# Kernel optimization log

Hardware: AMD Instinct MI355X
Metric: run time of the kernel (lower is better)

The kernel has to match this reference:

```python
import jax, jax.numpy as jnp
import numpy as np

K = 16            # neighbors
QUERY_CHUNK = 256 # SE is applied per chunk of this many query points (matches torch loop)
EPS = 1e-5        # BatchNorm eps (eval mode, running stats)


def bn(x, g, b, m, v):
    # eval-mode batchnorm over last axis (channel-last layout here)
    return (x - m) * (g / jnp.sqrt(v + EPS)) + b


def setup_inputs() -> dict:
    key = jax.random.key(0)
    ks = jax.random.split(key, 16)
    B, Cin, N = 4, 128, 4096
    H, Cout = 128, 256
    se_h = Cout // 4
    r = lambda k, s, sc=1.0: jax.random.normal(k, s, jnp.float32) * sc
    return dict(
        x=r(ks[0], (B, Cin, N)),
        W_edge=r(ks[1], (H, 2 * Cin), 0.05),          # edge_mlp conv2d 1x1
        bn1_g=jnp.ones((H,), jnp.float32), bn1_b=jnp.zeros((H,), jnp.float32),
        bn1_m=r(ks[2], (H,), 0.1), bn1_v=jax.random.uniform(ks[3], (H,), jnp.float32) + 0.5,
        w_att=r(ks[4], (H,), 0.1),                     # att_conv (1,H,1,1)
        W_fuse=r(ks[5], (Cout, H), 0.05),              # fuse conv1d
        bn2_g=jnp.ones((Cout,), jnp.float32), bn2_b=jnp.zeros((Cout,), jnp.float32),
        bn2_m=r(ks[6], (Cout,), 0.1), bn2_v=jax.random.uniform(ks[7], (Cout,), jnp.float32) + 0.5,
        fc1_w=r(ks[8], (se_h, Cout), 0.05), fc1_b=jnp.zeros((se_h,), jnp.float32),
        fc2_w=r(ks[9], (Cout, se_h), 0.05), fc2_b=jnp.zeros((Cout,), jnp.float32),
        W_res=r(ks[10], (Cout, Cin), 0.05),            # res_conv conv1d (in!=out)
        bn3_g=jnp.ones((Cout,), jnp.float32), bn3_b=jnp.zeros((Cout,), jnp.float32),
        bn3_m=r(ks[11], (Cout,), 0.1), bn3_v=jax.random.uniform(ks[12], (Cout,), jnp.float32) + 0.5,
    )


def reference(x, W_edge, bn1_g, bn1_b, bn1_m, bn1_v, w_att,
              W_fuse, bn2_g, bn2_b, bn2_m, bn2_v,
              fc1_w, fc1_b, fc2_w, fc2_b,
              W_res, bn3_g, bn3_b, bn3_m, bn3_v):
    B, Cin, N = x.shape
    x_t = jnp.swapaxes(x, 1, 2)  # (B,N,Cin)

    # KNN on features (dynamic=False -> knn on x.transpose); squared euclidean
    # has the same ordering as torch.cdist(p=2).
    sq = jnp.sum(x_t * x_t, axis=-1)                               # (B,N)
    d2 = sq[:, :, None] + sq[:, None, :] - 2.0 * jnp.einsum('bnc,bmc->bnm', x_t, x_t)
    _, idx = jax.lax.top_k(-d2, K)                                  # (B,N,K) smallest dists

    neigh = jax.vmap(lambda p, i: p[i])(x_t, idx)                   # (B,N,K,Cin)
    center = jnp.broadcast_to(x_t[:, :, None, :], neigh.shape)      # (B,N,K,Cin)
    edge = jnp.concatenate([neigh - center, center], axis=-1)       # (B,N,K,2Cin)

    # edge_mlp: 1x1 conv + BN + ReLU
    h = jax.nn.relu(bn(jnp.einsum('bnkc,hc->bnkh', edge, W_edge),
                       bn1_g, bn1_b, bn1_m, bn1_v))                 # (B,N,K,H)

    # attention over neighbors
    att = jax.nn.softmax(jnp.einsum('bnkh,h->bnk', h, w_att), axis=-1)
    agg = jnp.einsum('bnkh,bnk->bnh', h, att)                       # (B,N,H)

    # fuse conv1d + BN + ReLU
    out = jax.nn.relu(bn(jnp.einsum('bnh,oh->bno', agg, W_fuse),
                         bn2_g, bn2_b, bn2_m, bn2_v))               # (B,N,Cout)

    # SE channel attention, applied per query chunk (matches torch loop semantics)
    Cout = out.shape[-1]
    nc = N // QUERY_CHUNK
    oc = out.reshape(B, nc, QUERY_CHUNK, Cout)
    s = oc.mean(axis=2)                                             # (B,nc,Cout)
    s = jax.nn.relu(jnp.einsum('bmc,hc->bmh', s, fc1_w) + fc1_b)
    s = jax.nn.sigmoid(jnp.einsum('bmh,ch->bmc', s, fc2_w) + fc2_b)
    out = (oc * s[:, :, None, :]).reshape(B, N, Cout)

    # residual projection (in_channels != out_channels)
    res = bn(jnp.einsum('bnc,oc->bno', x_t, W_res), bn3_g, bn3_b, bn3_m, bn3_v)
    out = out + res
    return jnp.swapaxes(out, 1, 2)                                  # (B,Cout,N)
```

## Files before the change

kernel.cpp:

```cpp
#include <hip/hip_runtime.h>
#include <cstddef>

typedef __bf16 bf16;
typedef __bf16 bf16x8 __attribute__((ext_vector_type(8)));
typedef float  f32x4  __attribute__((ext_vector_type(4)));
typedef unsigned short u16;
typedef unsigned long long u64;

#define MFMA16x16(a, b, c) __builtin_amdgcn_mfma_f32_16x16x32_bf16((a), (b), (c), 0, 0, 0)

namespace {
constexpr int BB   = 4;
constexpr int CIN  = 128;
constexpr int NPT  = 4096;
constexpr int KNBR = 16;
constexpr int HED  = 128;
constexpr int COUT = 256;
}

__device__ __forceinline__ unsigned int ord_f32(float f) {
  unsigned int b = __float_as_uint(f);
  return b ^ (0x80000000u | (unsigned int)((int)b >> 31));
}
__device__ __forceinline__ u64 mk_key(float d, int m) {
  return ((u64)ord_f32(d) << 32) | (unsigned int)m;
}

__device__ __forceinline__ void sort16(u64* k) {
  #pragma unroll
  for (int sz = 2; sz <= 16; sz <<= 1) {
    #pragma unroll
    for (int st = sz >> 1; st > 0; st >>= 1) {
      #pragma unroll
      for (int i = 0; i < 16; ++i) {
        const int j = i ^ st;
        if (j > i) {
          const bool up = ((i & sz) == 0);
          const u64 a = k[i], c = k[j];
          const bool sw = up ? (a > c) : (a < c);
          k[i] = sw ? c : a;
          k[j] = sw ? a : c;
        }
      }
    }
  }
}

__device__ __forceinline__ void merge16(u64* R, const u64* B) {
  u64 t[16];
  #pragma unroll
  for (int i = 0; i < 16; ++i) {
    const u64 a = R[i], c = B[15 - i];
    t[i] = (a < c) ? a : c;
  }
  #pragma unroll
  for (int st = 8; st > 0; st >>= 1) {
    #pragma unroll
    for (int i = 0; i < 16; ++i) {
      const int j = i ^ st;
      if (j > i) {
        const u64 a = t[i], c = t[j];
        const bool sw = a > c;
        t[i] = sw ? c : a;
        t[j] = sw ? a : c;
      }
    }
  }
  #pragma unroll
  for (int i = 0; i < 16; ++i) R[i] = t[i];
}

__global__ __launch_bounds__(256) void k_wconv(const float* __restrict__ We,
                                               const float* __restrict__ Wf,
                                               const float* __restrict__ Wr,
                                               bf16* __restrict__ Web,
                                               bf16* __restrict__ Wfb,
                                               bf16* __restrict__ Wrb) {
  const int i = blockIdx.x * 256 + threadIdx.x;
  const int a = i >> 15;
  const int j = i & 32767;
  const float* src = (a == 0) ? We : (a == 1) ? Wf : Wr;
  bf16*        dst = (a == 0) ? Web : (a == 1) ? Wfb : Wrb;
  dst[j] = (bf16)src[j];
}

__global__ __launch_bounds__(256) void k_prep(const float* __restrict__ x,
                                              bf16* __restrict__ xh,
                                              bf16* __restrict__ xl,
                                              float* __restrict__ sq) {
  __shared__ __attribute__((aligned(16))) bf16 th[64][136];
  __shared__ __attribute__((aligned(16))) bf16 tl[64][136];
  __shared__ float sqp[4][64];
  const int tid = threadIdx.x;
  const int b   = blockIdx.x >> 6;
  const int n0  = (blockIdx.x & 63) << 6;
  const int nl  = tid & 63;
  const int cg  = tid >> 6;
  const float* xb = x + (size_t)b * CIN * NPT;
  float acc = 0.f;
  #pragma unroll
  for (int rep = 0; rep < 32; ++rep) {
    const int c = rep * 4 + cg;
    const float v = xb[(size_t)c * NPT + n0 + nl];
    const bf16 h = (bf16)v;
    const bf16 l = (bf16)(v - (float)h);
    acc += v * v;
    th[nl][c] = h;
    tl[nl][c] = l;
  }
  sqp[cg][nl] = acc;
  __syncthreads();
  bf16* xho = xh + ((size_t)b * NPT + n0) * CIN;
  bf16* xlo = xl + ((size_t)b * NPT + n0) * CIN;
  #pragma unroll
  for (int rep = 0; rep < 32; ++rep) {
    const int e = rep * 256 + tid;
    const int r = e >> 7;
    const int c = e & 127;
    xho[(size_t)r * CIN + c] = th[r][c];
    xlo[(size_t)r * CIN + c] = tl[r][c];
  }
  if (tid < 64) {
    sq[b * NPT + n0 + tid] = sqp[0][tid] + sqp[1][tid] + sqp[2][tid] + sqp[3][tid];
  }
}

__global__ __launch_bounds__(256, 2) void k_knn(const bf16* __restrict__ xh,
                                                const bf16* __restrict__ xl,
                                                const float* __restrict__ sq,
                                                int* __restrict__ knn_idx) {
  __shared__ u64 Lk[32][258];
  const int tid  = threadIdx.x;
  const int w    = tid >> 6;
  const int lane = tid & 63;
  const int col  = lane & 15;
  const int quad = lane >> 4;
  const int b    = blockIdx.x >> 7;
  const int q0   = (blockIdx.x & 127) << 5;
  const bf16*  xhb = xh + (size_t)b * NPT * CIN;
  const bf16*  xlb = xl + (size_t)b * NPT * CIN;
  const float* sqb = sq + b * NPT;

  bf16x8 qh[2][4], ql[2][4];
  float sqn[2];
  #pragma unroll
  for (int t = 0; t < 2; ++t) {
    const bf16* qrh = xhb + (size_t)(q0 + t * 16 + col) * CIN + quad * 8;
    const bf16* qrl = xlb + (size_t)(q0 + t * 16 + col) * CIN + quad * 8;
    #pragma unroll
    for (int ks = 0; ks < 4; ++ks) {
      qh[t][ks] = *(const bf16x8*)(qrh + ks * 32);
      ql[t][ks] = *(const bf16x8*)(qrl + ks * 32);
    }
    sqn[t] = sqb[q0 + t * 16 + col];
  }

  u64 R0[16], R1[16];
  #pragma unroll
  for (int i = 0; i < 16; ++i) { R0[i] = ~0ull; R1[i] = ~0ull; }

  const int cbase = w << 10;
  for (int mt = 0; mt < 16; ++mt) {
    const int m0 = cbase + (mt << 6);
    u64 k0[16], k1[16];
    #pragma unroll
    for (int cb = 0; cb < 4; ++cb) {
      const bf16* crh = xhb + (size_t)(m0 + cb * 16 + col) * CIN + quad * 8;
      const bf16* crl = xlb + (size_t)(m0 + cb * 16 + col) * CIN + quad * 8;
      f32x4 a0 = {0.f, 0.f, 0.f, 0.f};
      f32x4 a1 = {0.f, 0.f, 0.f, 0.f};
      #pragma unroll
      for (int ks = 0; ks < 4; ++ks) {
        const bf16x8 ch_ = *(const bf16x8*)(crh + ks * 32);
        const bf16x8 cl_ = *(const bf16x8*)(crl + ks * 32);
        a0 = MFMA16x16(cl_, qh[0][ks], a0);
        a0 = MFMA16x16(ch_, ql[0][ks], a0);
        a0 = MFMA16x16(ch_, qh[0][ks], a0);
        a1 = MFMA16x16(cl_, qh[1][ks], a1);
        a1 = MFMA16x16(ch_, ql[1][ks], a1);
        a1 = MFMA16x16(ch_, qh[1][ks], a1);
      }
      const f32x4 sqm = *(const f32x4*)(sqb + m0 + cb * 16 + quad * 4);
      #pragma unroll
      for (int r = 0; r < 4; ++r) {
        const int m = m0 + cb * 16 + quad * 4 + r;
        k0[cb * 4 + r] = mk_key((sqn[0] + sqm[r]) - 2.0f * a0[r], m);
        k1[cb * 4 + r] = mk_key((sqn[1] + sqm[r]) - 2.0f * a1[r], m);
      }
    }
    sort16(k0); merge16(R0, k0);
    sort16(k1); merge16(R1, k1);
  }

  {
    const int run = (w << 2) | quad;
    const int qA = col;
    const int qB = 16 | col;
    #pragma unroll
    for (int i = 0; i < 16; ++i) {
      Lk[qA][run * 16 + i] = R0[i];
      Lk[qB][run * 16 + i] = R1[i];
    }
  }
  __syncthreads();

  #pragma unroll
  for (int half = 8; half >= 1; half >>= 1) {
    u64 A[16], Bv[16];
    const bool act = tid < 32 * half;
    const int q = tid / half;
    const int j = tid % half;
    if (act) {
      #pragma unroll
      for (int i = 0; i < 16; ++i) {
        A[i]  = Lk[q][(2 * j) * 16 + i];
        Bv[i] = Lk[q][(2 * j + 1) * 16 + i];
      }
    }
    __syncthreads();
    if (act) {
      merge16(A, Bv);
      #pragma unroll
      for (int i = 0; i < 16; ++i) Lk[q][j * 16 + i] = A[i];
    }
    __syncthreads();
  }

  if (tid < 32) {
    int* op = knn_idx + (size_t)(b * NPT + q0 + tid) * KNBR;
    #pragma unroll
    for (int i = 0; i < 16; ++i) op[i] = (int)(Lk[tid][i] & 0xFFFFFFFFull);
  }
}

__global__ __launch_bounds__(256) void k_edge(const bf16* __restrict__ xh,
                                              const bf16* __restrict__ xl,
                                              const int* __restrict__ knn_idx,
                                              const bf16* __restrict__ We,
                                              const float* __restrict__ g1, const float* __restrict__ b1,
                                              const float* __restrict__ m1, const float* __restrict__ v1,
                                              const float* __restrict__ watt,
                                              bf16* __restrict__ agg) {
  __shared__ __attribute__((aligned(16))) bf16 Ew[4][16][264];
  __shared__ float s1[HED], t1[HED], wat[HED];
  const int tid  = threadIdx.x;
  const int w    = tid >> 6;
  const int lane = tid & 63;
  const int col  = lane & 15;
  const int quad = lane >> 4;
  if (tid < HED) {
    const float ss = g1[tid] / sqrtf(v1[tid] + 1e-5f);
    s1[tid] = ss;
    t1[tid] = b1[tid] - m1[tid] * ss;
    wat[tid] = watt[tid];
  }
  __syncthreads();
  const int gw = blockIdx.x * 4 + w;
  for (int it = 0; it < 4; ++it) {
    const int p = gw * 4 + it;
    const int b = p >> 12;
    const int n = p & 4095;
    const bf16* xhb = xh + (size_t)b * NPT * CIN;
    const bf16* xlb = xl + (size_t)b * NPT * CIN;
    const int my = knn_idx[(size_t)p * KNBR + col];
    const int m  = __shfl(my, lane >> 2);
    const int sub = lane & 3;
    const int kn  = lane >> 2;
    const bf16* nh = xhb + (size_t)m * CIN + sub * 32;
    const bf16* nl_ = xlb + (size_t)m * CIN + sub * 32;
    const bf16* ch = xhb + (size_t)n * CIN + sub * 32;
    const bf16* cl = xlb + (size_t)n * CIN + sub * 32;
    #pragma unroll
    for (int j = 0; j < 4; ++j) {
      const bf16x8 nhv = *(const bf16x8*)(nh + j * 8);
      const bf16x8 nlv = *(const bf16x8*)(nl_ + j * 8);
      const bf16x8 chv = *(const bf16x8*)(ch + j * 8);
      const bf16x8 clv = *(const bf16x8*)(cl + j * 8);
      bf16x8 dv, cv;
      #pragma unroll
      for (int e = 0; e < 8; ++e) {
        const float nf = (float)nhv[e] + (float)nlv[e];
        const float cf = (float)chv[e] + (float)clv[e];
        dv[e] = (bf16)(nf - cf);
        cv[e] = (bf16)cf;
      }
      *(bf16x8*)&Ew[w][kn][sub * 32 + j * 8]       = dv;
      *(bf16x8*)&Ew[w][kn][128 + sub * 32 + j * 8] = cv;
    }
    __syncthreads();
    const f32x4 zero4 = {0.f, 0.f, 0.f, 0.f};
    f32x4 acc[8];
    #pragma unroll
    for (int hb = 0; hb < 8; ++hb) acc[hb] = zero4;
    #pragma unroll
    for (int ks = 0; ks < 8; ++ks) {
      const bf16x8 af = *(const bf16x8*)&Ew[w][col][ks * 32 + quad * 8];
      #pragma unroll
      for (int hb = 0; hb < 8; ++hb) {
        const bf16x8 bfv = *(const bf16x8*)(We + (size_t)(hb * 16 + col) * 256 + ks * 32 + quad * 8);
        acc[hb] = MFMA16x16(af, bfv, acc[hb]);
      }
    }
    float h[8][4];
    float lg[4] = {0.f, 0.f, 0.f, 0.f};
    #pragma unroll
    for (int hb = 0; hb < 8; ++hb) {
      const int hc = hb * 16 + col;
      const float ss = s1[hc], tt = t1[hc], ww = wat[hc];
      #pragma unroll
      for (int r = 0; r < 4; ++r) {
        const float hv = fmaxf(acc[hb][r] * ss + tt, 0.f);
        h[hb][r] = hv;
        lg[r] += hv * ww;
      }
    }
    #pragma unroll
    for (int r = 0; r < 4; ++r) {
      float vv = lg[r];
      vv += __shfl_xor(vv, 1);
      vv += __shfl_xor(vv, 2);
      vv += __shfl_xor(vv, 4);
      vv += __shfl_xor(vv, 8);
      lg[r] = vv;
    }
    float mx = fmaxf(fmaxf(lg[0], lg[1]), fmaxf(lg[2], lg[3]));
    mx = fmaxf(mx, __shfl_xor(mx, 16));
    mx = fmaxf(mx, __shfl_xor(mx, 32));
    float ex[4];
    float sm = 0.f;
    #pragma unroll
    for (int r = 0; r < 4; ++r) { ex[r] = expf(lg[r] - mx); sm += ex[r]; }
    sm += __shfl_xor(sm, 16);
    sm += __shfl_xor(sm, 32);
    const float inv = 1.0f / sm;
    float ag[8];
    #pragma unroll
    for (int hb = 0; hb < 8; ++hb) {
      float a = h[hb][0] * ex[0] + h[hb][1] * ex[1] + h[hb][2] * ex[2] + h[hb][3] * ex[3];
      a += __shfl_xor(a, 16);
      a += __shfl_xor(a, 32);
      ag[hb] = a * inv;
    }
    if (quad == 0) {
      bf16* ao = agg + (size_t)p * HED;
      #pragma unroll
      for (int hb = 0; hb < 8; ++hb) ao[hb * 16 + col] = (bf16)ag[hb];
    }
    __syncthreads();
  }
}

__global__ __launch_bounds__(256) void k_fuse(const bf16* __restrict__ agg,
                                              const bf16* __restrict__ Wf,
                                              const float* __restrict__ g2, const float* __restrict__ b2,
                                              const float* __restrict__ m2, const float* __restrict__ v2,
                                              bf16* __restrict__ outp) {
  const int tid  = threadIdx.x;
  const int w    = tid >> 6;
  const int lane = tid & 63;
  const int col  = lane & 15;
  const int quad = lane >> 4;
  const int p0   = (blockIdx.x * 4 + w) * 16;
  bf16x8 afr[4];
  const bf16* arow = agg + (size_t)(p0 + col) * HED + quad * 8;
  #pragma unroll
  for (int ks = 0; ks < 4; ++ks) afr[ks] = *(const bf16x8*)(arow + ks * 32);
  #pragma unroll
  for (int ob = 0; ob < 16; ++ob) {
    f32x4 acc = {0.f, 0.f, 0.f, 0.f};
    const bf16* brow = Wf + (size_t)(ob * 16 + col) * HED + quad * 8;
    #pragma unroll
    for (int ks = 0; ks < 4; ++ks)
      acc = MFMA16x16(afr[ks], *(const bf16x8*)(brow + ks * 32), acc);
    const int o = ob * 16 + col;
    const float ss = g2[o] / sqrtf(v2[o] + 1e-5f);
    const float tt = b2[o] - m2[o] * ss;
    #pragma unroll
    for (int r = 0; r < 4; ++r) {
      outp[(size_t)(p0 + quad * 4 + r) * COUT + o] = (bf16)fmaxf(acc[r] * ss + tt, 0.f);
    }
  }
}

__global__ __launch_bounds__(256) void k_se(const bf16* __restrict__ outp,
                                            const float* __restrict__ f1w, const float* __restrict__ f1b,
                                            const float* __restrict__ f2w, const float* __restrict__ f2b,
                                            float* __restrict__ sse) {
  __shared__ float mean_s[COUT];
  __shared__ float h1[64];
  const int bc  = blockIdx.x;
  const int tid = threadIdx.x;
  const bf16* base = outp + (size_t)bc * 256 * COUT;
  float s = 0.f;
  for (int p2 = 0; p2 < 256; ++p2) s += (float)base[(size_t)p2 * COUT + tid];
  mean_s[tid] = s * (1.0f / 256.0f);
  __syncthreads();
  if (tid < 64) {
    float a = f1b[tid];
    for (int c = 0; c < COUT; ++c) a += f1w[tid * COUT + c] * mean_s[c];
    h1[tid] = fmaxf(a, 0.f);
  }
  __syncthreads();
  float a = f2b[tid];
  #pragma unroll
  for (int j = 0; j < 64; ++j) a += f2w[tid * 64 + j] * h1[j];
  sse[(size_t)bc * COUT + tid] = 1.0f / (1.0f + expf(-a));
}

__global__ __launch_bounds__(256) void k_final(const bf16* __restrict__ xh,
                                               const bf16* __restrict__ Wr,
                                               const float* __restrict__ g3, const float* __restrict__ b3,
                                               const float* __restrict__ m3, const float* __restrict__ v3,
                                               const bf16* __restrict__ outp,
                                               const float* __restrict__ sse,
                                               float* __restrict__ out) {
  const int tid  = threadIdx.x;
  const int w    = tid >> 6;
  const int lane = tid & 63;
  const int col  = lane & 15;
  const int quad = lane >> 4;
  const int p0   = (blockIdx.x * 4 + w) * 16;
  const int b    = p0 >> 12;
  const int n0l  = p0 & 4095;
  bf16x8 afr[4];
  const bf16* arow = xh + (size_t)(p0 + col) * CIN + quad * 8;
  #pragma unroll
  for (int ks = 0; ks < 4; ++ks) afr[ks] = *(const bf16x8*)(arow + ks * 32);
  const float* scb = sse + (size_t)(b * 16 + (n0l >> 8)) * COUT;
  #pragma unroll
  for (int ob = 0; ob < 16; ++ob) {
    f32x4 acc = {0.f, 0.f, 0.f, 0.f};
    const bf16* brow = Wr + (size_t)(ob * 16 + col) * CIN + quad * 8;
    #pragma unroll
    for (int ks = 0; ks < 4; ++ks)
      acc = MFMA16x16(afr[ks], *(const bf16x8*)(brow + ks * 32), acc);
    const int o = ob * 16 + col;
    const float ss = g3[o] / sqrtf(v3[o] + 1e-5f);
    const float tt = b3[o] - m3[o] * ss;
    const float sc = scb[o];
    f32x4 pk;
    #pragma unroll
    for (int r = 0; r < 4; ++r) {
      const float res = acc[r] * ss + tt;
      pk[r] = (float)outp[(size_t)(p0 + quad * 4 + r) * COUT + o] * sc + res;
    }
    float* op = out + (size_t)(b * COUT + o) * NPT + n0l + quad * 4;
    *(f32x4*)op = pk;
  }
}

extern "C" void kernel_launch(void* const* d_in, const int* in_sizes, int n_in,
                              void* d_out, int out_size, void* d_ws, size_t ws_size,
                              hipStream_t stream) {
  (void)in_sizes; (void)n_in; (void)out_size; (void)ws_size;
  const float* x    = (const float*)d_in[0];
  const float* We   = (const float*)d_in[1];
  const float* g1   = (const float*)d_in[2];
  const float* b1   = (const float*)d_in[3];
  const float* m1   = (const float*)d_in[4];
  const float* v1   = (const float*)d_in[5];
  const float* watt = (const float*)d_in[6];
  const float* Wf   = (const float*)d_in[7];
  const float* g2   = (const float*)d_in[8];
  const float* b2   = (const float*)d_in[9];
  const float* m2   = (const float*)d_in[10];
  const float* v2   = (const float*)d_in[11];
  const float* f1w  = (const float*)d_in[12];
  const float* f1b  = (const float*)d_in[13];
  const float* f2w  = (const float*)d_in[14];
  const float* f2b  = (const float*)d_in[15];
  const float* Wr   = (const float*)d_in[16];
  const float* g3   = (const float*)d_in[17];
  const float* b3   = (const float*)d_in[18];
  const float* m3   = (const float*)d_in[19];
  const float* v3   = (const float*)d_in[20];

  char* ws = (char*)d_ws;
  size_t off = 0;
  bf16*  xth  = (bf16*)(ws + off);  off += (size_t)BB * NPT * CIN * 2;
  bf16*  xtl  = (bf16*)(ws + off);  off += (size_t)BB * NPT * CIN * 2;
  float* sq   = (float*)(ws + off); off += (size_t)BB * NPT * 4;
  int*   idxp = (int*)(ws + off);   off += (size_t)BB * NPT * KNBR * 4;
  bf16*  aggp = (bf16*)(ws + off);  off += (size_t)BB * NPT * HED * 2;
  bf16*  outp = (bf16*)(ws + off);  off += (size_t)BB * NPT * COUT * 2;
  float* ssep = (float*)(ws + off); off += (size_t)BB * 16 * COUT * 4;
  bf16*  Web  = (bf16*)(ws + off);  off += (size_t)HED * 2 * CIN * 2;
  bf16*  Wfb  = (bf16*)(ws + off);  off += (size_t)COUT * HED * 2;
  bf16*  Wrb  = (bf16*)(ws + off);  off += (size_t)COUT * CIN * 2;

  float* out = (float*)d_out;

  k_wconv<<<384, 256, 0, stream>>>(We, Wf, Wr, Web, Wfb, Wrb);
  k_prep<<<256, 256, 0, stream>>>(x, xth, xtl, sq);
  k_knn<<<512, 256, 0, stream>>>(xth, xtl, sq, idxp);
  k_edge<<<1024, 256, 0, stream>>>(xth, xtl, idxp, Web, g1, b1, m1, v1, watt, aggp);
  k_fuse<<<256, 256, 0, stream>>>(aggp, Wfb, g2, b2, m2, v2, outp);
  k_se<<<64, 256, 0, stream>>>(outp, f1w, f1b, f2w, f2b, ssep);
  k_final<<<256, 256, 0, stream>>>(xth, Wrb, g3, b3, m3, v3, outp, ssep, out);
}
```

Before: 430.0 us.

## Merge KNN runs via wave shuffles and build edge MFMA fragments in registers

In the KNN kernel, the per-lane top-16 lists are now merged across quads with cross-lane shuffles instead of through shared memory. The shared buffer shrinks to one run per wave, so the final block-level merge becomes a single serial pass by 32 threads with no repeated barriers. Launch bounds rise to 4 blocks per CU, and the first tile initialises the running list directly instead of merging against sentinels. In the edge kernel, the gathered edge features are loaded straight into MFMA A-fragment registers, which removes the shared staging buffer and its barriers but raises register pressure and makes neighbour loads less coalesced.

Result: slower. 727.1 us (+69.1%).

```diff
diff --git a/kernel.cpp b/kernel.cpp
--- a/kernel.cpp
+++ b/kernel.cpp
@@ -125,11 +125,11 @@
   }
 }
 
-__global__ __launch_bounds__(256, 2) void k_knn(const bf16* __restrict__ xh,
+__global__ __launch_bounds__(256, 4) void k_knn(const bf16* __restrict__ xh,
                                                 const bf16* __restrict__ xl,
                                                 const float* __restrict__ sq,
                                                 int* __restrict__ knn_idx) {
-  __shared__ u64 Lk[32][258];
+  __shared__ u64 Lk[32][65];
   const int tid  = threadIdx.x;
   const int w    = tid >> 6;
   const int lane = tid & 63;
@@ -156,9 +156,6 @@
   }
 
   u64 R0[16], R1[16];
-  #pragma unroll
-  for (int i = 0; i < 16; ++i) { R0[i] = ~0ull; R1[i] = ~0ull; }
-
   const int cbase = w << 10;
   for (int mt = 0; mt < 16; ++mt) {
     const int m0 = cbase + (mt << 6);
@@ -188,48 +185,54 @@
         k1[cb * 4 + r] = mk_key((sqn[1] + sqm[r]) - 2.0f * a1[r], m);
       }
     }
-    sort16(k0); merge16(R0, k0);
-    sort16(k1); merge16(R1, k1);
+    sort16(k0);
+    sort16(k1);
+    if (mt == 0) {
+      #pragma unroll
+      for (int i = 0; i < 16; ++i) { R0[i] = k0[i]; R1[i] = k1[i]; }
+    } else {
+      merge16(R0, k0);
+      merge16(R1, k1);
+    }
   }
 
   {
-    const int run = (w << 2) | quad;
-    const int qA = col;
-    const int qB = 16 | col;
+    u64 P[16];
+    #pragma unroll
+    for (int i = 0; i < 16; ++i) P[i] = __shfl_xor((u64)R0[i], 16);
+    merge16(R0, P);
+    #pragma unroll
+    for (int i = 0; i < 16; ++i) P[i] = __shfl_xor((u64)R0[i], 32);
+    merge16(R0, P);
+    #pragma unroll
+    for (int i = 0; i < 16; ++i) P[i] = __shfl_xor((u64)R1[i], 16);
+    merge16(R1, P);
+    #pragma unroll
+    for (int i = 0; i < 16; ++i) P[i] = __shfl_xor((u64)R1[i], 32);
+    merge16(R1, P);
+  }
+  if (quad == 0) {
     #pragma unroll
     for (int i = 0; i < 16; ++i) {
-      Lk[qA][run * 16 + i] = R0[i];
-      Lk[qB][run * 16 + i] = R1[i];
+      Lk[col][w * 16 + i]        = R0[i];
+      Lk[16 | col][w * 16 + i]   = R1[i];
     }
   }
   __syncthreads();
 
-  #pragma unroll
-  for (int half = 8; half >= 1; half >>= 1) {
+  if (tid < 32) {
     u64 A[16], Bv[16];
-    const bool act = tid < 32 * half;
-    const int q = tid / half;
-    const int j = tid % half;
-    if (act) {
-      #pragma unroll
-      for (int i = 0; i < 16; ++i) {
-        A[i]  = Lk[q][(2 * j) * 16 + i];
-        Bv[i] = Lk[q][(2 * j + 1) * 16 + i];
-      }
-    }
-    __syncthreads();
-    if (act) {
+    #pragma unroll
+    for (int i = 0; i < 16; ++i) A[i] = Lk[tid][i];
+    #pragma unroll
+    for (int run = 1; run < 4; ++run) {
+      #pragma unroll
+      for (int i = 0; i < 16; ++i) Bv[i] = Lk[tid][run * 16 + i];
       merge16(A, Bv);
-      #pragma unroll
-      for (int i = 0; i < 16; ++i) Lk[q][j * 16 + i] = A[i];
-    }
-    __syncthreads();
-  }
-
-  if (tid < 32) {
+    }
     int* op = knn_idx + (size_t)(b * NPT + q0 + tid) * KNBR;
     #pragma unroll
-    for (int i = 0; i < 16; ++i) op[i] = (int)(Lk[tid][i] & 0xFFFFFFFFull);
+    for (int i = 0; i < 16; ++i) op[i] = (int)(A[i] & 0xFFFFFFFFull);
   }
 }
 
@@ -241,7 +244,6 @@
                                               const float* __restrict__ m1, const float* __restrict__ v1,
                                               const float* __restrict__ watt,
                                               bf16* __restrict__ agg) {
-  __shared__ __attribute__((aligned(16))) bf16 Ew[4][16][264];
   __shared__ float s1[HED], t1[HED], wat[HED];
   const int tid  = threadIdx.x;
   const int w    = tid >> 6;
@@ -262,20 +264,18 @@
     const int n = p & 4095;
     const bf16* xhb = xh + (size_t)b * NPT * CIN;
     const bf16* xlb = xl + (size_t)b * NPT * CIN;
-    const int my = knn_idx[(size_t)p * KNBR + col];
-    const int m  = __shfl(my, lane >> 2);
-    const int sub = lane & 3;
-    const int kn  = lane >> 2;
-    const bf16* nh = xhb + (size_t)m * CIN + sub * 32;
-    const bf16* nl_ = xlb + (size_t)m * CIN + sub * 32;
-    const bf16* ch = xhb + (size_t)n * CIN + sub * 32;
-    const bf16* cl = xlb + (size_t)n * CIN + sub * 32;
-    #pragma unroll
-    for (int j = 0; j < 4; ++j) {
-      const bf16x8 nhv = *(const bf16x8*)(nh + j * 8);
-      const bf16x8 nlv = *(const bf16x8*)(nl_ + j * 8);
-      const bf16x8 chv = *(const bf16x8*)(ch + j * 8);
-      const bf16x8 clv = *(const bf16x8*)(cl + j * 8);
+    const int m = knn_idx[(size_t)p * KNBR + col];
+    const bf16* nh  = xhb + (size_t)m * CIN + quad * 8;
+    const bf16* nl_ = xlb + (size_t)m * CIN + quad * 8;
+    const bf16* ch  = xhb + (size_t)n * CIN + quad * 8;
+    const bf16* cl  = xlb + (size_t)n * CIN + quad * 8;
+    bf16x8 af[8];
+    #pragma unroll
+    for (int ks = 0; ks < 4; ++ks) {
+      const bf16x8 nhv = *(const bf16x8*)(nh + ks * 32);
+      const bf16x8 nlv = *(const bf16x8*)(nl_ + ks * 32);
+      const bf16x8 chv = *(const bf16x8*)(ch + ks * 32);
+      const bf16x8 clv = *(const bf16x8*)(cl + ks * 32);
       bf16x8 dv, cv;
       #pragma unroll
       for (int e = 0; e < 8; ++e) {
@@ -284,21 +284,19 @@
         dv[e] = (bf16)(nf - cf);
         cv[e] = (bf16)cf;
       }
-      *(bf16x8*)&Ew[w][kn][sub * 32 + j * 8]       = dv;
-      *(bf16x8*)&Ew[w][kn][128 + sub * 32 + j * 8] = cv;
-    }
-    __syncthreads();
+      af[ks]     = dv;
+      af[4 + ks] = cv;
+    }
     const f32x4 zero4 = {0.f, 0.f, 0.f, 0.f};
     f32x4 acc[8];
     #pragma unroll
     for (int hb = 0; hb < 8; ++hb) acc[hb] = zero4;
     #pragma unroll
     for (int ks = 0; ks < 8; ++ks) {
-      const bf16x8 af = *(const bf16x8*)&Ew[w][col][ks * 32 + quad * 8];
       #pragma unroll
       for (int hb = 0; hb < 8; ++hb) {
         const bf16x8 bfv = *(const bf16x8*)(We + (size_t)(hb * 16 + col) * 256 + ks * 32 + quad * 8);
-        acc[hb] = MFMA16x16(af, bfv, acc[hb]);
+        acc[hb] = MFMA16x16(af[ks], bfv, acc[hb]);
       }
     }
     float h[8][4];
@@ -346,7 +344,6 @@
       #pragma unroll
       for (int hb = 0; hb < 8; ++hb) ao[hb * 16 + col] = (bf16)ag[hb];
     }
-    __syncthreads();
   }
 }
 
```
